# Optimization experiments

Measured on AMD Instinct MI355X. Metric: run time of the kernel, lower is better.

## Reference

```python
import jax, jax.numpy as jnp
import numpy as np

N_NODES = 100000
N_EDGES = 3200000
D_IN = 128
D_OUT = 128


def setup_inputs() -> dict:
    key = jax.random.key(0)
    k1, k2, k3, k4, k5 = jax.random.split(key, 5)
    x = jax.random.normal(k1, (N_NODES, D_IN), dtype=jnp.float32)
    adj_rows = jax.random.randint(k2, (N_EDGES,), 0, N_NODES, dtype=jnp.int64)
    adj_cols = jax.random.randint(k3, (N_EDGES,), 0, N_NODES, dtype=jnp.int64)
    adj_vals = jax.random.uniform(k4, (N_EDGES,), dtype=jnp.float32)
    # torch Linear weight has shape (dim_out, dim_in)
    W = jax.random.normal(k5, (D_OUT, D_IN), dtype=jnp.float32) * (1.0 / np.sqrt(D_IN))
    return {"x": x, "adj_rows": adj_rows, "adj_cols": adj_cols, "adj_vals": adj_vals, "W": W}


def reference(x, adj_rows, adj_cols, adj_vals, W):
    # h = Linear(x) with no bias: x @ W^T  -> [N, D_OUT]
    h = x @ W.T
    # sparse.mm(adjacency, h): out[r] = sum_e vals[e] * h[cols[e]] for edges with rows[e]==r
    msgs = adj_vals[:, None] * h[adj_cols]           # [E, D_OUT]
    agg = jax.ops.segment_sum(msgs, adj_rows, num_segments=N_NODES)
    return jax.nn.relu(agg)
```

## Files before the change

kernel.cpp:

```cpp
#include <hip/hip_runtime.h>
#include <stdint.h>

typedef unsigned short u16;
typedef unsigned int u32;
typedef unsigned long long u64;
typedef __attribute__((ext_vector_type(8))) short short8;
typedef __attribute__((ext_vector_type(4))) float floatx4;

#define DIM 128
#define DIM2 64
#define NBK 2048
#define NB_SH 6
#define AGG_NB 64
#define AGG_CAP 2560
#define SC_C 8192
#define HIST_C 4096

__device__ __forceinline__ u32 f32_to_bf16_rne(float f) {
  u32 u = __float_as_uint(f);
  u32 r = u + 0x7fffu + ((u >> 16) & 1u);
  return r >> 16;
}
__device__ __forceinline__ float bf16_to_f32(u32 u) { return __uint_as_float(u << 16); }
__device__ __forceinline__ u32 pack2bf16(float a, float b) {
  return f32_to_bf16_rne(a) | (f32_to_bf16_rne(b) << 16);
}

union FragU {
  u32 d[4];
  short8 s;
};

__global__ __launch_bounds__(256) void gemm_mfma(const float* __restrict__ x,
                                                 const float* __restrict__ W,
                                                 u16* __restrict__ h, int N) {
  __shared__ u32 Wl[DIM * DIM2];
  int tid = threadIdx.x;
#pragma unroll
  for (int i = 0; i < 8; ++i) {
    int ga = tid + 256 * i;
    int o = ga >> 4, g = ga & 15;
    const float* src = W + (size_t)o * DIM + g * 8;
    floatx4 f0 = *(const floatx4*)src;
    floatx4 f1 = *(const floatx4*)(src + 4);
    int slot = (g + o) & 15;
    u32* dst = &Wl[o * DIM2 + slot * 4];
    dst[0] = pack2bf16(f0.x, f0.y);
    dst[1] = pack2bf16(f0.z, f0.w);
    dst[2] = pack2bf16(f1.x, f1.y);
    dst[3] = pack2bf16(f1.z, f1.w);
  }
  __syncthreads();

  int lane = tid & 63;
  int wave = tid >> 6;
  int m = lane & 15;
  int kg = lane >> 4;
  int ntile = (N + 63) >> 6;

  for (int t = blockIdx.x; t < ntile; t += 256) {
    int nodeBase = t * 64 + wave * 16;
    if (nodeBase >= N) continue;

    short8 a[4];
    const float* xr = x + (size_t)(nodeBase + m) * DIM + kg * 8;
#pragma unroll
    for (int kt = 0; kt < 4; ++kt) {
      floatx4 f0 = *(const floatx4*)(xr + kt * 32);
      floatx4 f1 = *(const floatx4*)(xr + kt * 32 + 4);
      FragU fu;
      fu.d[0] = pack2bf16(f0.x, f0.y);
      fu.d[1] = pack2bf16(f0.z, f0.w);
      fu.d[2] = pack2bf16(f1.x, f1.y);
      fu.d[3] = pack2bf16(f1.z, f1.w);
      a[kt] = fu.s;
    }

#pragma unroll
    for (int ot = 0; ot < 8; ++ot) {
      int o = ot * 16 + m;
      floatx4 acc = {0.f, 0.f, 0.f, 0.f};
#pragma unroll
      for (int kt = 0; kt < 4; ++kt) {
        int slot = (kt * 4 + kg + o) & 15;
        short8 b = *(short8*)&Wl[o * DIM2 + slot * 4];
        acc = __builtin_amdgcn_mfma_f32_16x16x32_bf16(a[kt], b, acc, 0, 0, 0);
      }
#pragma unroll
      for (int r = 0; r < 4; ++r) {
        int node = nodeBase + kg * 4 + r;
        h[(size_t)node * DIM + ot * 16 + m] = (u16)f32_to_bf16_rne(acc[r]);
      }
    }
  }
}

__global__ void zero_kernel(int* __restrict__ p, int n) {
  int i = blockIdx.x * blockDim.x + threadIdx.x;
  if (i < n) p[i] = 0;
}

__device__ __forceinline__ void scan2048(u32* cnt, u32* excl, u32* wtot) {
  int tid = threadIdx.x, lane = tid & 63, wave = tid >> 6;
  u32 c[8], sum = 0;
#pragma unroll
  for (int k = 0; k < 8; ++k) {
    c[k] = cnt[tid * 8 + k];
    sum += c[k];
  }
  u32 inc = sum;
#pragma unroll
  for (int d = 1; d < 64; d <<= 1) {
    u32 t = __shfl_up(inc, d, 64);
    if (lane >= d) inc += t;
  }
  if (lane == 63) wtot[wave] = inc;
  __syncthreads();
  u32 wbase = 0;
  for (int w = 0; w < wave; ++w) wbase += wtot[w];
  u32 run = wbase + inc - sum;
#pragma unroll
  for (int k = 0; k < 8; ++k) {
    excl[tid * 8 + k] = run;
    run += c[k];
  }
  __syncthreads();
}

__global__ __launch_bounds__(256) void bucket_hist(const int* __restrict__ rows,
                                                   int* __restrict__ bhist, int E, int B) {
  __shared__ u32 hist[NBK];
  int tid = threadIdx.x;
  for (int b = tid; b < NBK; b += 256) hist[b] = 0;
  __syncthreads();
  int base = blockIdx.x * HIST_C;
  for (int j = tid; j < HIST_C; j += 256) {
    int e = base + j;
    if (e < E) atomicAdd(&hist[((u32)rows[e]) >> NB_SH], 1u);
  }
  __syncthreads();
  for (int b = tid; b < B; b += 256) {
    u32 c = hist[b];
    if (c) atomicAdd(&bhist[b], (int)c);
  }
}

__global__ __launch_bounds__(256) void bucket_scan(const int* __restrict__ bhist,
                                                   int* __restrict__ bbase,
                                                   int* __restrict__ bptr) {
  __shared__ u32 cnt[NBK], excl[NBK], wtot[4];
  int tid = threadIdx.x;
  for (int b = tid; b < NBK; b += 256) cnt[b] = (u32)bhist[b];
  __syncthreads();
  scan2048(cnt, excl, wtot);
  for (int b = tid; b < NBK; b += 256) {
    bbase[b] = (int)excl[b];
    bptr[b] = (int)excl[b];
  }
}

__global__ __launch_bounds__(256) void bin_scatter(const int* __restrict__ rows,
                                                   const int* __restrict__ cols,
                                                   const float* __restrict__ vals,
                                                   int* __restrict__ bptr,
                                                   u32* __restrict__ bcol,
                                                   u16* __restrict__ bval, int E) {
  __shared__ u32 hist[NBK];
  __shared__ u32 starts[NBK];
  __shared__ u32 gbase[NBK];
  __shared__ u32 wtot[4];
  __shared__ u32 s_rec[SC_C];
  int tid = threadIdx.x;
  int base = blockIdx.x * SC_C;
  int tot = min(SC_C, E - base);

  for (int b = tid; b < NBK; b += 256) hist[b] = 0;
  __syncthreads();
  for (int j = tid; j < tot; j += 256) {
    atomicAdd(&hist[((u32)rows[base + j]) >> NB_SH], 1u);
  }
  __syncthreads();
  scan2048(hist, starts, wtot);
  for (int b = tid; b < NBK; b += 256) {
    u32 c = hist[b];
    gbase[b] = c ? (u32)atomicAdd(&bptr[b], (int)c) : 0u;
    hist[b] = starts[b];
  }
  __syncthreads();
  for (int j = tid; j < tot; j += 256) {
    u32 r = (u32)rows[base + j];
    u32 bk = r >> NB_SH;
    u32 p = atomicAdd(&hist[bk], 1u);
    s_rec[p] = (bk << 19) | ((r & 63u) << 13) | (u32)j;
  }
  __syncthreads();
  for (int i = tid; i < tot; i += 256) {
    u32 rec = s_rec[i];
    u32 bk = rec >> 19;
    u32 nl = (rec >> 13) & 63u;
    int e = base + (int)(rec & 8191u);
    u32 d = gbase[bk] + ((u32)i - starts[bk]);
    bcol[d] = (nl << 26) | ((u32)cols[e] << 8);
    bval[d] = (u16)f32_to_bf16_rne(vals[e]);
  }
}

__global__ __launch_bounds__(256) void agg_bucket(const int* __restrict__ bhist,
                                                  const int* __restrict__ bbase,
                                                  const u32* __restrict__ bcol,
                                                  const u16* __restrict__ bval,
                                                  const u32* __restrict__ h,
                                                  float* __restrict__ out, int N) {
  __shared__ u64 s_rec[AGG_CAP];
  __shared__ u32 cnt[AGG_NB], excl[AGG_NB], ptr[AGG_NB];
  int tid = threadIdx.x, lane = tid & 63, wave = tid >> 6;
  int b = blockIdx.x;
  int base = bbase[b], T = bhist[b];
  int nodeBase = b << NB_SH;
  int lane4 = lane * 4;
  const char* hb = (const char*)h;

  if (T <= AGG_CAP) {
    if (tid < AGG_NB) cnt[tid] = 0;
    __syncthreads();
    u32 rlo[10], rv[10];
#pragma unroll
    for (int k = 0; k < 10; ++k) {
      int j = tid + 256 * k;
      rlo[k] = 0;
      rv[k] = 0;
      if (j < T) {
        rlo[k] = bcol[base + j];
        rv[k] = bval[base + j];
        atomicAdd(&cnt[rlo[k] >> 26], 1u);
      }
    }
    __syncthreads();
    if (tid < 64) {
      u32 c = cnt[tid], inc = c;
#pragma unroll
      for (int d = 1; d < 64; d <<= 1) {
        u32 t = __shfl_up(inc, d, 64);
        if (lane >= d) inc += t;
      }
      excl[tid] = inc - c;
      ptr[tid] = inc - c;
    }
    __syncthreads();
#pragma unroll
    for (int k = 0; k < 10; ++k) {
      int j = tid + 256 * k;
      if (j < T) {
        u32 p = atomicAdd(&ptr[rlo[k] >> 26], 1u);
        s_rec[p] = ((u64)(rv[k] << 16) << 32) | rlo[k];
      }
    }
    __syncthreads();
    int wbeg = (int)excl[wave * 16];
    int wend = (int)ptr[wave * 16 + 15];
    float a0 = 0.f, a1 = 0.f;
    int curn = -1;
    for (int e = wbeg; e < wend; e += 8) {
      u32 lo8[8];
      float v8[8];
      u32 hd[8];
#pragma unroll
      for (int g = 0; g < 8; ++g) {
        int ee = e + g;
        bool act = ee < wend;
        u64 r = s_rec[act ? ee : (wend - 1)];
        lo8[g] = (u32)r;
        v8[g] = act ? __uint_as_float((u32)(r >> 32)) : 0.f;
      }
#pragma unroll
      for (int g = 0; g < 8; ++g) {
        hd[g] = *(const u32*)(hb + ((lo8[g] & 0x01FFFF00u) + lane4));
      }
#pragma unroll
      for (int g = 0; g < 8; ++g) {
        int nid = __builtin_amdgcn_readfirstlane((int)(lo8[g] >> 26));
        if (nid != curn) {
          if (curn >= 0) {
            float2 o = make_float2(fmaxf(a0, 0.f), fmaxf(a1, 0.f));
            *(float2*)(out + (size_t)(nodeBase + curn) * DIM + 2 * lane) = o;
          }
          curn = nid;
          a0 = 0.f;
          a1 = 0.f;
        }
        float v = v8[g];
        a0 += v * bf16_to_f32(hd[g] & 0xffffu);
        a1 += v * bf16_to_f32(hd[g] >> 16);
      }
    }
    if (curn >= 0) {
      float2 o = make_float2(fmaxf(a0, 0.f), fmaxf(a1, 0.f));
      *(float2*)(out + (size_t)(nodeBase + curn) * DIM + 2 * lane) = o;
    }
    for (int nn = 0; nn < 16; ++nn) {
      int nl = wave * 16 + nn;
      int node = nodeBase + nl;
      if (cnt[nl] == 0 && node < N) {
        *(float2*)(out + (size_t)node * DIM + 2 * lane) = make_float2(0.f, 0.f);
      }
    }
  } else {
    for (int nn = 0; nn < 16; ++nn) {
      int nl = wave * 16 + nn;
      int node = nodeBase + nl;
      if (node >= N) continue;
      float a0 = 0.f, a1 = 0.f;
      for (int e = 0; e < T; ++e) {
        u32 lo = bcol[base + e];
        if ((int)(lo >> 26) == nl) {
          u32 d = *(const u32*)(hb + ((lo & 0x01FFFF00u) + lane4));
          float v = bf16_to_f32(bval[base + e]);
          a0 += v * bf16_to_f32(d & 0xffffu);
          a1 += v * bf16_to_f32(d >> 16);
        }
      }
      *(float2*)(out + (size_t)node * DIM + 2 * lane) =
          make_float2(fmaxf(a0, 0.f), fmaxf(a1, 0.f));
    }
  }
}

extern "C" void kernel_launch(void* const* d_in, const int* in_sizes, int n_in,
                              void* d_out, int out_size, void* d_ws, size_t ws_size,
                              hipStream_t stream) {
  const float* x    = (const float*)d_in[0];
  const int*   rows = (const int*)d_in[1];
  const int*   cols = (const int*)d_in[2];
  const float* vals = (const float*)d_in[3];
  const float* W    = (const float*)d_in[4];

  const int N = in_sizes[0] / DIM;
  const int E = in_sizes[1];
  const int B = (N + AGG_NB - 1) / AGG_NB;

  char* wsb = (char*)d_ws;
  size_t o = 0;
  u16* h = (u16*)wsb;                    o += (size_t)N * DIM * sizeof(u16);
  int* bhist = (int*)(wsb + o);          o += (size_t)NBK * 4;
  int* bbase = (int*)(wsb + o);          o += (size_t)NBK * 4;
  int* bptr  = (int*)(wsb + o);          o += (size_t)NBK * 4;
  u32* bcol  = (u32*)(wsb + o);          o += (size_t)E * 4;
  u16* bval  = (u16*)(wsb + o);          o += (size_t)E * 2;

  const int nhist = (E + HIST_C - 1) / HIST_C;
  const int nsc = (E + SC_C - 1) / SC_C;

  zero_kernel<<<(NBK + 255) / 256, 256, 0, stream>>>(bhist, NBK);
  gemm_mfma<<<256, 256, 0, stream>>>(x, W, h, N);
  bucket_hist<<<nhist, 256, 0, stream>>>(rows, bhist, E, B);
  bucket_scan<<<1, 256, 0, stream>>>(bhist, bbase, bptr);
  bin_scatter<<<nsc, 256, 0, stream>>>(rows, cols, vals, bptr, bcol, bval, E);
  agg_bucket<<<B, 256, 0, stream>>>(bhist, bbase, bcol, bval, (const u32*)h,
                                    (float*)d_out, N);
}
```

Measured before the change: 344.9 us.

## Replace global bucket histogram/scan with per-block local sort plus directory

Removes the zero, global histogram and global scan kernels. Each scatter block now sorts its chunk locally by bucket and writes it contiguously, along with a per-block directory of (offset, count) per bucket. The aggregation kernel rebuilds its bucket's edge list by scanning that directory and binary-searching segments. This cuts kernel launches and global atomics, but each aggregation block must now read nsc directory entries and gather from many small, scattered segments.

```diff
diff --git a/kernel.cpp b/kernel.cpp
--- a/kernel.cpp
+++ b/kernel.cpp
@@ -9,12 +9,12 @@
 
 #define DIM 128
 #define DIM2 64
-#define NBK 2048
+#define NBK 1792
+#define NBK_PT 7
 #define NB_SH 6
 #define AGG_NB 64
 #define AGG_CAP 2560
 #define SC_C 8192
-#define HIST_C 4096
 
 __device__ __forceinline__ u32 f32_to_bf16_rne(float f) {
   u32 u = __float_as_uint(f);
@@ -95,17 +95,12 @@
   }
 }
 
-__global__ void zero_kernel(int* __restrict__ p, int n) {
-  int i = blockIdx.x * blockDim.x + threadIdx.x;
-  if (i < n) p[i] = 0;
-}
-
-__device__ __forceinline__ void scan2048(u32* cnt, u32* excl, u32* wtot) {
+__device__ __forceinline__ void scan_nbk(u32* cnt, u32* excl, u32* wtot) {
   int tid = threadIdx.x, lane = tid & 63, wave = tid >> 6;
-  u32 c[8], sum = 0;
-#pragma unroll
-  for (int k = 0; k < 8; ++k) {
-    c[k] = cnt[tid * 8 + k];
+  u32 c[NBK_PT], sum = 0;
+#pragma unroll
+  for (int k = 0; k < NBK_PT; ++k) {
+    c[k] = cnt[tid * NBK_PT + k];
     sum += c[k];
   }
   u32 inc = sum;
@@ -120,58 +115,27 @@
   for (int w = 0; w < wave; ++w) wbase += wtot[w];
   u32 run = wbase + inc - sum;
 #pragma unroll
-  for (int k = 0; k < 8; ++k) {
-    excl[tid * 8 + k] = run;
+  for (int k = 0; k < NBK_PT; ++k) {
+    excl[tid * NBK_PT + k] = run;
     run += c[k];
   }
   __syncthreads();
 }
 
-__global__ __launch_bounds__(256) void bucket_hist(const int* __restrict__ rows,
-                                                   int* __restrict__ bhist, int E, int B) {
-  __shared__ u32 hist[NBK];
-  int tid = threadIdx.x;
-  for (int b = tid; b < NBK; b += 256) hist[b] = 0;
-  __syncthreads();
-  int base = blockIdx.x * HIST_C;
-  for (int j = tid; j < HIST_C; j += 256) {
-    int e = base + j;
-    if (e < E) atomicAdd(&hist[((u32)rows[e]) >> NB_SH], 1u);
-  }
-  __syncthreads();
-  for (int b = tid; b < B; b += 256) {
-    u32 c = hist[b];
-    if (c) atomicAdd(&bhist[b], (int)c);
-  }
-}
-
-__global__ __launch_bounds__(256) void bucket_scan(const int* __restrict__ bhist,
-                                                   int* __restrict__ bbase,
-                                                   int* __restrict__ bptr) {
-  __shared__ u32 cnt[NBK], excl[NBK], wtot[4];
-  int tid = threadIdx.x;
-  for (int b = tid; b < NBK; b += 256) cnt[b] = (u32)bhist[b];
-  __syncthreads();
-  scan2048(cnt, excl, wtot);
-  for (int b = tid; b < NBK; b += 256) {
-    bbase[b] = (int)excl[b];
-    bptr[b] = (int)excl[b];
-  }
-}
-
-__global__ __launch_bounds__(256) void bin_scatter(const int* __restrict__ rows,
-                                                   const int* __restrict__ cols,
-                                                   const float* __restrict__ vals,
-                                                   int* __restrict__ bptr,
-                                                   u32* __restrict__ bcol,
-                                                   u16* __restrict__ bval, int E) {
+__global__ __launch_bounds__(256) void sort_scatter(const int* __restrict__ rows,
+                                                    const int* __restrict__ cols,
+                                                    const float* __restrict__ vals,
+                                                    u32* __restrict__ bcol,
+                                                    u16* __restrict__ bval,
+                                                    u32* __restrict__ dir, int E, int B) {
   __shared__ u32 hist[NBK];
   __shared__ u32 starts[NBK];
-  __shared__ u32 gbase[NBK];
   __shared__ u32 wtot[4];
-  __shared__ u32 s_rec[SC_C];
+  __shared__ u32 s_lo[SC_C];
+  __shared__ u16 s_val[SC_C];
   int tid = threadIdx.x;
-  int base = blockIdx.x * SC_C;
+  int wg = blockIdx.x;
+  int base = wg * SC_C;
   int tot = min(SC_C, E - base);
 
   for (int b = tid; b < NBK; b += 256) hist[b] = 0;
@@ -180,58 +144,82 @@
     atomicAdd(&hist[((u32)rows[base + j]) >> NB_SH], 1u);
   }
   __syncthreads();
-  scan2048(hist, starts, wtot);
-  for (int b = tid; b < NBK; b += 256) {
-    u32 c = hist[b];
-    gbase[b] = c ? (u32)atomicAdd(&bptr[b], (int)c) : 0u;
-    hist[b] = starts[b];
-  }
+  scan_nbk(hist, starts, wtot);
+  for (int b = tid; b < NBK; b += 256) hist[b] = starts[b];
   __syncthreads();
   for (int j = tid; j < tot; j += 256) {
     u32 r = (u32)rows[base + j];
     u32 bk = r >> NB_SH;
     u32 p = atomicAdd(&hist[bk], 1u);
-    s_rec[p] = (bk << 19) | ((r & 63u) << 13) | (u32)j;
+    s_lo[p] = ((r & 63u) << 26) | ((u32)cols[base + j] << 8);
+    s_val[p] = (u16)f32_to_bf16_rne(vals[base + j]);
   }
   __syncthreads();
   for (int i = tid; i < tot; i += 256) {
-    u32 rec = s_rec[i];
-    u32 bk = rec >> 19;
-    u32 nl = (rec >> 13) & 63u;
-    int e = base + (int)(rec & 8191u);
-    u32 d = gbase[bk] + ((u32)i - starts[bk]);
-    bcol[d] = (nl << 26) | ((u32)cols[e] << 8);
-    bval[d] = (u16)f32_to_bf16_rne(vals[e]);
-  }
-}
-
-__global__ __launch_bounds__(256) void agg_bucket(const int* __restrict__ bhist,
-                                                  const int* __restrict__ bbase,
-                                                  const u32* __restrict__ bcol,
+    bcol[(size_t)base + i] = s_lo[i];
+    bval[(size_t)base + i] = s_val[i];
+  }
+  for (int b = tid; b < B; b += 256) {
+    dir[(size_t)wg * B + b] = (starts[b] << 16) | (hist[b] - starts[b]);
+  }
+}
+
+__global__ __launch_bounds__(256) void agg_bucket(const u32* __restrict__ bcol,
                                                   const u16* __restrict__ bval,
+                                                  const u32* __restrict__ dir,
                                                   const u32* __restrict__ h,
-                                                  float* __restrict__ out, int N) {
+                                                  float* __restrict__ out, int N,
+                                                  int nsc, int B) {
   __shared__ u64 s_rec[AGG_CAP];
-  __shared__ u32 cnt[AGG_NB], excl[AGG_NB], ptr[AGG_NB];
+  __shared__ u32 segdir[512], segdst[512];
+  __shared__ u32 cnt[AGG_NB], excl[AGG_NB], ptr[AGG_NB], wtot[4];
   int tid = threadIdx.x, lane = tid & 63, wave = tid >> 6;
   int b = blockIdx.x;
-  int base = bbase[b], T = bhist[b];
   int nodeBase = b << NB_SH;
   int lane4 = lane * 4;
   const char* hb = (const char*)h;
 
+  for (int w = tid; w < nsc; w += 256) segdir[w] = dir[(size_t)w * B + b];
+  if (tid < AGG_NB) cnt[tid] = 0;
+  __syncthreads();
+  {
+    int e0 = 2 * tid, e1 = e0 + 1;
+    u32 c0 = (e0 < nsc) ? (segdir[e0] & 0xffffu) : 0u;
+    u32 c1 = (e1 < nsc) ? (segdir[e1] & 0xffffu) : 0u;
+    u32 s = c0 + c1, inc = s;
+#pragma unroll
+    for (int d = 1; d < 64; d <<= 1) {
+      u32 t = __shfl_up(inc, d, 64);
+      if (lane >= d) inc += t;
+    }
+    if (lane == 63) wtot[wave] = inc;
+    __syncthreads();
+    u32 wbase = 0;
+    for (int w = 0; w < wave; ++w) wbase += wtot[w];
+    u32 ex = wbase + inc - s;
+    segdst[e0] = ex;
+    segdst[e1] = ex + c0;
+    __syncthreads();
+  }
+  int T = (int)(wtot[0] + wtot[1] + wtot[2] + wtot[3]);
+
   if (T <= AGG_CAP) {
-    if (tid < AGG_NB) cnt[tid] = 0;
-    __syncthreads();
     u32 rlo[10], rv[10];
 #pragma unroll
     for (int k = 0; k < 10; ++k) {
-      int j = tid + 256 * k;
+      int g = tid + 256 * k;
       rlo[k] = 0;
       rv[k] = 0;
-      if (j < T) {
-        rlo[k] = bcol[base + j];
-        rv[k] = bval[base + j];
+      if (g < T) {
+        int lo = 0, hi = nsc - 1;
+        while (lo < hi) {
+          int mid = (lo + hi + 1) >> 1;
+          if (segdst[mid] <= (u32)g) lo = mid; else hi = mid - 1;
+        }
+        u32 dv = segdir[lo];
+        u32 src = (u32)lo * SC_C + (dv >> 16) + ((u32)g - segdst[lo]);
+        rlo[k] = bcol[src];
+        rv[k] = bval[src];
         atomicAdd(&cnt[rlo[k] >> 26], 1u);
       }
     }
@@ -249,8 +237,8 @@
     __syncthreads();
 #pragma unroll
     for (int k = 0; k < 10; ++k) {
-      int j = tid + 256 * k;
-      if (j < T) {
+      int g = tid + 256 * k;
+      if (g < T) {
         u32 p = atomicAdd(&ptr[rlo[k] >> 26], 1u);
         s_rec[p] = ((u64)(rv[k] << 16) << 32) | rlo[k];
       }
@@ -310,13 +298,18 @@
       int node = nodeBase + nl;
       if (node >= N) continue;
       float a0 = 0.f, a1 = 0.f;
-      for (int e = 0; e < T; ++e) {
-        u32 lo = bcol[base + e];
-        if ((int)(lo >> 26) == nl) {
-          u32 d = *(const u32*)(hb + ((lo & 0x01FFFF00u) + lane4));
-          float v = bf16_to_f32(bval[base + e]);
-          a0 += v * bf16_to_f32(d & 0xffffu);
-          a1 += v * bf16_to_f32(d >> 16);
+      for (int w = 0; w < nsc; ++w) {
+        u32 dv = segdir[w];
+        int sc = (int)(dv & 0xffffu);
+        u32 so = dv >> 16;
+        for (int r = 0; r < sc; ++r) {
+          u32 lo = bcol[(size_t)w * SC_C + so + r];
+          if ((int)(lo >> 26) == nl) {
+            u32 d = *(const u32*)(hb + ((lo & 0x01FFFF00u) + lane4));
+            float v = bf16_to_f32(bval[(size_t)w * SC_C + so + r]);
+            a0 += v * bf16_to_f32(d & 0xffffu);
+            a1 += v * bf16_to_f32(d >> 16);
+          }
         }
       }
       *(float2*)(out + (size_t)node * DIM + 2 * lane) =
@@ -337,24 +330,17 @@
   const int N = in_sizes[0] / DIM;
   const int E = in_sizes[1];
   const int B = (N + AGG_NB - 1) / AGG_NB;
+  const int nsc = (E + SC_C - 1) / SC_C;
 
   char* wsb = (char*)d_ws;
   size_t o = 0;
-  u16* h = (u16*)wsb;                    o += (size_t)N * DIM * sizeof(u16);
-  int* bhist = (int*)(wsb + o);          o += (size_t)NBK * 4;
-  int* bbase = (int*)(wsb + o);          o += (size_t)NBK * 4;
-  int* bptr  = (int*)(wsb + o);          o += (size_t)NBK * 4;
-  u32* bcol  = (u32*)(wsb + o);          o += (size_t)E * 4;
-  u16* bval  = (u16*)(wsb + o);          o += (size_t)E * 2;
-
-  const int nhist = (E + HIST_C - 1) / HIST_C;
-  const int nsc = (E + SC_C - 1) / SC_C;
-
-  zero_kernel<<<(NBK + 255) / 256, 256, 0, stream>>>(bhist, NBK);
+  u16* h = (u16*)wsb;            o += (size_t)N * DIM * sizeof(u16);
+  u32* bcol = (u32*)(wsb + o);   o += (size_t)nsc * SC_C * sizeof(u32);
+  u16* bval = (u16*)(wsb + o);   o += (size_t)nsc * SC_C * sizeof(u16);
+  u32* dir  = (u32*)(wsb + o);   o += (size_t)nsc * B * sizeof(u32);
+
   gemm_mfma<<<256, 256, 0, stream>>>(x, W, h, N);
-  bucket_hist<<<nhist, 256, 0, stream>>>(rows, bhist, E, B);
-  bucket_scan<<<1, 256, 0, stream>>>(bhist, bbase, bptr);
-  bin_scatter<<<nsc, 256, 0, stream>>>(rows, cols, vals, bptr, bcol, bval, E);
-  agg_bucket<<<B, 256, 0, stream>>>(bhist, bbase, bcol, bval, (const u32*)h,
-                                    (float*)d_out, N);
-}
+  sort_scatter<<<nsc, 256, 0, stream>>>(rows, cols, vals, bcol, bval, dir, E, B);
+  agg_bucket<<<B, 256, 0, stream>>>(bcol, bval, dir, (const u32*)h,
+                                    (float*)d_out, N, nsc, B);
+}
```

Result: no change. 342.7 us (-0.6%).

## Launch one GEMM tile per block, widen bin_scatter to 512 threads, split agg records

Applied to the files above, without the earlier changes.

The GEMM stops looping over tiles in a 256-block grid and instead launches one 64-node tile per block, giving far more blocks to cover the device. bin_scatter moves to 512 threads with an inline 4-per-thread scan. It folds the global base and the local start into one offset, which removes the gbase array and cuts shared memory. agg_bucket keeps its sorted edge records as separate u32 and u16 shared arrays instead of packed u64, shrinking LDS use, at the cost of two LDS reads per record.

```diff
diff --git a/kernel.cpp b/kernel.cpp
--- a/kernel.cpp
+++ b/kernel.cpp
@@ -54,43 +54,39 @@
 
   int lane = tid & 63;
   int wave = tid >> 6;
+  int nodeBase = (blockIdx.x * 4 + wave) * 16;
+  if (nodeBase >= N) return;
   int m = lane & 15;
   int kg = lane >> 4;
-  int ntile = (N + 63) >> 6;
-
-  for (int t = blockIdx.x; t < ntile; t += 256) {
-    int nodeBase = t * 64 + wave * 16;
-    if (nodeBase >= N) continue;
-
-    short8 a[4];
-    const float* xr = x + (size_t)(nodeBase + m) * DIM + kg * 8;
+
+  short8 a[4];
+  const float* xr = x + (size_t)(nodeBase + m) * DIM + kg * 8;
+#pragma unroll
+  for (int kt = 0; kt < 4; ++kt) {
+    floatx4 f0 = *(const floatx4*)(xr + kt * 32);
+    floatx4 f1 = *(const floatx4*)(xr + kt * 32 + 4);
+    FragU fu;
+    fu.d[0] = pack2bf16(f0.x, f0.y);
+    fu.d[1] = pack2bf16(f0.z, f0.w);
+    fu.d[2] = pack2bf16(f1.x, f1.y);
+    fu.d[3] = pack2bf16(f1.z, f1.w);
+    a[kt] = fu.s;
+  }
+
+#pragma unroll
+  for (int ot = 0; ot < 8; ++ot) {
+    int o = ot * 16 + m;
+    floatx4 acc = {0.f, 0.f, 0.f, 0.f};
 #pragma unroll
     for (int kt = 0; kt < 4; ++kt) {
-      floatx4 f0 = *(const floatx4*)(xr + kt * 32);
-      floatx4 f1 = *(const floatx4*)(xr + kt * 32 + 4);
-      FragU fu;
-      fu.d[0] = pack2bf16(f0.x, f0.y);
-      fu.d[1] = pack2bf16(f0.z, f0.w);
-      fu.d[2] = pack2bf16(f1.x, f1.y);
-      fu.d[3] = pack2bf16(f1.z, f1.w);
-      a[kt] = fu.s;
-    }
-
-#pragma unroll
-    for (int ot = 0; ot < 8; ++ot) {
-      int o = ot * 16 + m;
-      floatx4 acc = {0.f, 0.f, 0.f, 0.f};
-#pragma unroll
-      for (int kt = 0; kt < 4; ++kt) {
-        int slot = (kt * 4 + kg + o) & 15;
-        short8 b = *(short8*)&Wl[o * DIM2 + slot * 4];
-        acc = __builtin_amdgcn_mfma_f32_16x16x32_bf16(a[kt], b, acc, 0, 0, 0);
-      }
-#pragma unroll
-      for (int r = 0; r < 4; ++r) {
-        int node = nodeBase + kg * 4 + r;
-        h[(size_t)node * DIM + ot * 16 + m] = (u16)f32_to_bf16_rne(acc[r]);
-      }
+      int slot = (kt * 4 + kg + o) & 15;
+      short8 b = *(short8*)&Wl[o * DIM2 + slot * 4];
+      acc = __builtin_amdgcn_mfma_f32_16x16x32_bf16(a[kt], b, acc, 0, 0, 0);
+    }
+#pragma unroll
+    for (int r = 0; r < 4; ++r) {
+      int node = nodeBase + kg * 4 + r;
+      h[(size_t)node * DIM + ot * 16 + m] = (u16)f32_to_bf16_rne(acc[r]);
     }
   }
 }
@@ -159,7 +155,7 @@
   }
 }
 
-__global__ __launch_bounds__(256) void bin_scatter(const int* __restrict__ rows,
+__global__ __launch_bounds__(512) void bin_scatter(const int* __restrict__ rows,
                                                    const int* __restrict__ cols,
                                                    const float* __restrict__ vals,
                                                    int* __restrict__ bptr,
@@ -167,39 +163,62 @@
                                                    u16* __restrict__ bval, int E) {
   __shared__ u32 hist[NBK];
   __shared__ u32 starts[NBK];
-  __shared__ u32 gbase[NBK];
-  __shared__ u32 wtot[4];
+  __shared__ u32 wtot[8];
   __shared__ u32 s_rec[SC_C];
-  int tid = threadIdx.x;
+  int tid = threadIdx.x, lane = tid & 63, wv = tid >> 6;
   int base = blockIdx.x * SC_C;
   int tot = min(SC_C, E - base);
 
-  for (int b = tid; b < NBK; b += 256) hist[b] = 0;
-  __syncthreads();
-  for (int j = tid; j < tot; j += 256) {
+  for (int b = tid; b < NBK; b += 512) hist[b] = 0;
+  __syncthreads();
+  for (int j = tid; j < tot; j += 512) {
     atomicAdd(&hist[((u32)rows[base + j]) >> NB_SH], 1u);
   }
   __syncthreads();
-  scan2048(hist, starts, wtot);
-  for (int b = tid; b < NBK; b += 256) {
+  {
+    u32 c[4], sum = 0;
+#pragma unroll
+    for (int k = 0; k < 4; ++k) {
+      c[k] = hist[tid * 4 + k];
+      sum += c[k];
+    }
+    u32 inc = sum;
+#pragma unroll
+    for (int d = 1; d < 64; d <<= 1) {
+      u32 t = __shfl_up(inc, d, 64);
+      if (lane >= d) inc += t;
+    }
+    if (lane == 63) wtot[wv] = inc;
+    __syncthreads();
+    u32 wbase = 0;
+    for (int w = 0; w < wv; ++w) wbase += wtot[w];
+    u32 run = wbase + inc - sum;
+#pragma unroll
+    for (int k = 0; k < 4; ++k) {
+      starts[tid * 4 + k] = run;
+      run += c[k];
+    }
+    __syncthreads();
+  }
+  for (int b = tid; b < NBK; b += 512) {
     u32 c = hist[b];
-    gbase[b] = c ? (u32)atomicAdd(&bptr[b], (int)c) : 0u;
-    hist[b] = starts[b];
-  }
-  __syncthreads();
-  for (int j = tid; j < tot; j += 256) {
+    u32 gb = c ? (u32)atomicAdd(&bptr[b], (int)c) : 0u;
+    hist[b] = gb - starts[b];
+  }
+  __syncthreads();
+  for (int j = tid; j < tot; j += 512) {
     u32 r = (u32)rows[base + j];
     u32 bk = r >> NB_SH;
-    u32 p = atomicAdd(&hist[bk], 1u);
+    u32 p = atomicAdd(&starts[bk], 1u);
     s_rec[p] = (bk << 19) | ((r & 63u) << 13) | (u32)j;
   }
   __syncthreads();
-  for (int i = tid; i < tot; i += 256) {
+  for (int i = tid; i < tot; i += 512) {
     u32 rec = s_rec[i];
     u32 bk = rec >> 19;
     u32 nl = (rec >> 13) & 63u;
     int e = base + (int)(rec & 8191u);
-    u32 d = gbase[bk] + ((u32)i - starts[bk]);
+    u32 d = hist[bk] + (u32)i;
     bcol[d] = (nl << 26) | ((u32)cols[e] << 8);
     bval[d] = (u16)f32_to_bf16_rne(vals[e]);
   }
@@ -211,7 +230,8 @@
                                                   const u16* __restrict__ bval,
                                                   const u32* __restrict__ h,
                                                   float* __restrict__ out, int N) {
-  __shared__ u64 s_rec[AGG_CAP];
+  __shared__ u32 s_lo[AGG_CAP];
+  __shared__ u16 s_v[AGG_CAP];
   __shared__ u32 cnt[AGG_NB], excl[AGG_NB], ptr[AGG_NB];
   int tid = threadIdx.x, lane = tid & 63, wave = tid >> 6;
   int b = blockIdx.x;
@@ -226,12 +246,12 @@
     u32 rlo[10], rv[10];
 #pragma unroll
     for (int k = 0; k < 10; ++k) {
-      int j = tid + 256 * k;
+      int g = tid + 256 * k;
       rlo[k] = 0;
       rv[k] = 0;
-      if (j < T) {
-        rlo[k] = bcol[base + j];
-        rv[k] = bval[base + j];
+      if (g < T) {
+        rlo[k] = bcol[base + g];
+        rv[k] = bval[base + g];
         atomicAdd(&cnt[rlo[k] >> 26], 1u);
       }
     }
@@ -249,10 +269,11 @@
     __syncthreads();
 #pragma unroll
     for (int k = 0; k < 10; ++k) {
-      int j = tid + 256 * k;
-      if (j < T) {
+      int g = tid + 256 * k;
+      if (g < T) {
         u32 p = atomicAdd(&ptr[rlo[k] >> 26], 1u);
-        s_rec[p] = ((u64)(rv[k] << 16) << 32) | rlo[k];
+        s_lo[p] = rlo[k];
+        s_v[p] = (u16)rv[k];
       }
     }
     __syncthreads();
@@ -268,9 +289,9 @@
       for (int g = 0; g < 8; ++g) {
         int ee = e + g;
         bool act = ee < wend;
-        u64 r = s_rec[act ? ee : (wend - 1)];
-        lo8[g] = (u32)r;
-        v8[g] = act ? __uint_as_float((u32)(r >> 32)) : 0.f;
+        int idx = act ? ee : (wend - 1);
+        lo8[g] = s_lo[idx];
+        v8[g] = act ? bf16_to_f32((u32)s_v[idx]) : 0.f;
       }
 #pragma unroll
       for (int g = 0; g < 8; ++g) {
@@ -351,10 +372,10 @@
   const int nsc = (E + SC_C - 1) / SC_C;
 
   zero_kernel<<<(NBK + 255) / 256, 256, 0, stream>>>(bhist, NBK);
-  gemm_mfma<<<256, 256, 0, stream>>>(x, W, h, N);
+  gemm_mfma<<<(N + 63) / 64, 256, 0, stream>>>(x, W, h, N);
   bucket_hist<<<nhist, 256, 0, stream>>>(rows, bhist, E, B);
   bucket_scan<<<1, 256, 0, stream>>>(bhist, bbase, bptr);
-  bin_scatter<<<nsc, 256, 0, stream>>>(rows, cols, vals, bptr, bcol, bval, E);
+  bin_scatter<<<nsc, 512, 0, stream>>>(rows, cols, vals, bptr, bcol, bval, E);
   agg_bucket<<<B, 256, 0, stream>>>(bhist, bbase, bcol, bval, (const u32*)h,
                                     (float*)d_out, N);
 }
```

After: 373.4 us. 1.08x slower.
